# Kernel optimization log

Hardware: AMD Instinct MI355X
Metric: run time of the kernel (lower is better)

Reference implementation:

```python
import jax, jax.numpy as jnp
import numpy as np
import math

C = 384; HQ = 8; HKV = 2; HD = C // HQ; R = 4; L = 4; E = 4; CAPF = 1.25; SCALE = 1.0 / R


def _ln(x, g, b):
    m = jnp.mean(x, -1, keepdims=True)
    v = jnp.mean((x - m) ** 2, -1, keepdims=True)
    return (x - m) * jax.lax.rsqrt(v + 1e-5) * g + b


def _lora(h, W, A, B):
    # base linear (no bias) + low-rank LoRA delta, scale = alpha/r = 0.25
    return h @ W + ((h @ A.T) @ B.T) * SCALE


def _rope(x, cos, sin):
    xe = x[..., 0::2]; xo = x[..., 1::2]
    return jnp.stack((xe * cos - xo * sin, xe * sin + xo * cos), axis=-1).reshape(x.shape)


def _forward(x, adapter_id, ln1_g, ln1_b, ln2_g, ln2_b,
             Wq, Aq, Bq, Wk, Ak, Bk, Wv, Av, Bv, Wo, Ao, Bo,
             Wr, br, W1, A1, B1, W2, A2, B2):
    B, T, _ = x.shape
    aid = adapter_id
    # ---- GQA attention with RoPE ----
    h = _ln(x, ln1_g, ln1_b)
    q = _lora(h, Wq, Aq[aid], Bq[aid]).reshape(B, T, HQ, HD).transpose(0, 2, 1, 3)
    k = _lora(h, Wk, Ak[aid], Bk[aid]).reshape(B, T, HKV, HD).transpose(0, 2, 1, 3)
    v = _lora(h, Wv, Av[aid], Bv[aid]).reshape(B, T, HKV, HD).transpose(0, 2, 1, 3)
    inv = 1.0 / (10000.0 ** (jnp.arange(0, HD, 2, dtype=x.dtype) / HD))
    ang = jnp.arange(T, dtype=x.dtype)[:, None] * inv  # [T, HD/2]
    cos = jnp.cos(ang); sin = jnp.sin(ang)
    q = _rope(q, cos, sin); k = _rope(k, cos, sin)
    rep = HQ // HKV
    k = jnp.repeat(k, rep, axis=1); v = jnp.repeat(v, rep, axis=1)
    s = jnp.einsum('bhqd,bhkd->bhqk', q, k) / math.sqrt(HD)
    causal = jnp.tril(jnp.ones((T, T), dtype=bool))
    s = jnp.where(causal, s, -jnp.inf)
    a = jax.nn.softmax(s, axis=-1)
    o = jnp.einsum('bhqk,bhkd->bhqd', a, v).transpose(0, 2, 1, 3).reshape(B, T, C)
    x = x + _lora(o, Wo, Ao[aid], Bo[aid])
    # ---- capacity-routed top-1 MoE with LoRA FFN experts ----
    flat = _ln(x, ln2_g, ln2_b).reshape(B * T, C)
    probs = jax.nn.softmax(flat @ Wr + br, axis=-1)   # [N, E]
    top1_val = jnp.max(probs, -1)
    top1_idx = jnp.argmax(probs, -1)
    onehot = jax.nn.one_hot(top1_idx, E, dtype=flat.dtype)
    pos = jnp.cumsum(onehot, axis=0) - 1.0            # slot within expert
    cap = int(math.ceil(CAPF * B * T / E))
    dispatch = (pos < cap).astype(flat.dtype) * onehot
    aux = jnp.sum(jnp.mean(probs, 0) * jnp.mean(dispatch, 0)) * E
    posi = pos.astype(jnp.int32)
    # fixed-capacity gather into per-expert buffers (dropped tokens -> slot cap)
    bufs = []
    for e in range(E):
        slot = jnp.where(dispatch[:, e] > 0, posi[:, e], cap)
        bufs.append(jnp.zeros((cap + 1, C), flat.dtype).at[slot].set(flat)[:cap])
    buf = jnp.stack(bufs)                              # [E, cap, C]
    a1 = A1[:, aid]; b1 = B1[:, aid]; a2 = A2[:, aid]; b2 = B2[:, aid]
    h1 = jnp.einsum('enc,eco->eno', buf, W1) \
        + jnp.einsum('enr,eor->eno', jnp.einsum('enc,erc->enr', buf, a1), b1) * SCALE
    h1 = jax.nn.relu(h1)
    o2 = jnp.einsum('enf,efo->eno', h1, W2) \
        + jnp.einsum('enr,eor->eno', jnp.einsum('enf,erf->enr', h1, a2), b2) * SCALE
    out_flat = jnp.zeros_like(flat)
    for e in range(E):
        g = dispatch[:, e] * top1_val                  # gate, zero for undisptched
        out_flat = out_flat + o2[e][jnp.clip(posi[:, e], 0, cap - 1)] * g[:, None]
    return x + out_flat.reshape(B, T, C), aux


def setup_inputs() -> dict:
    key = jax.random.key(0)
    ks = jax.random.split(key, 32)
    B, T = 4, 2048
    n = lambda i, shape, s=0.05: jax.random.normal(ks[i], shape, dtype=jnp.float32) * s
    inp = {
        'x': jax.random.normal(ks[0], (B, T, C), dtype=jnp.float32),
        'adapter_id': 0,
        'ln1_g': jnp.ones((C,), jnp.float32), 'ln1_b': jnp.zeros((C,), jnp.float32),
        'ln2_g': jnp.ones((C,), jnp.float32), 'ln2_b': jnp.zeros((C,), jnp.float32),
        'Wq': n(1, (C, HQ * HD)), 'Aq': n(2, (L, R, C), 0.1), 'Bq': n(3, (L, HQ * HD, R), 0.1),
        'Wk': n(4, (C, HKV * HD)), 'Ak': n(5, (L, R, C), 0.1), 'Bk': n(6, (L, HKV * HD, R), 0.1),
        'Wv': n(7, (C, HKV * HD)), 'Av': n(8, (L, R, C), 0.1), 'Bv': n(9, (L, HKV * HD, R), 0.1),
        'Wo': n(10, (C, C)), 'Ao': n(11, (L, R, C), 0.1), 'Bo': n(12, (L, C, R), 0.1),
        'Wr': n(13, (C, E)), 'br': jnp.zeros((E,), jnp.float32),
        'W1': n(14, (E, C, 4 * C)), 'A1': n(15, (E, L, R, C), 0.1), 'B1': n(16, (E, L, 4 * C, R), 0.1),
        'W2': n(17, (E, 4 * C, C)), 'A2': n(18, (E, L, R, 4 * C), 0.1), 'B2': n(19, (E, L, C, R), 0.1),
    }
    return inp


def reference(x, adapter_id, ln1_g, ln1_b, ln2_g, ln2_b,
              Wq, Aq, Bq, Wk, Ak, Bk, Wv, Av, Bv, Wo, Ao, Bo,
              Wr, br, W1, A1, B1, W2, A2, B2):
    return _forward(x, adapter_id, ln1_g, ln1_b, ln2_g, ln2_b,
                    Wq, Aq, Bq, Wk, Ak, Bk, Wv, Av, Bv, Wo, Ao, Bo,
                    Wr, br, W1, A1, B1, W2, A2, B2)
```

## Files before the change

kernel.cpp:

```cpp
#include <hip/hip_runtime.h>
#include <math.h>

#define NC   384
#define NHQ  8
#define NHKV 2
#define NR   4
#define NEXP 4
#define NB   4
#define NT   2048
#define NTOKENS 8192
#define NCAP 2560
#define NFF  1536
#define NQKV 576
#define LORA_SCALE 0.25f
#define L2E 1.4426950408889634f
#define QSCALE 0.14433756729740643f

#define OB_HSPLIT_HI ((size_t)0)
#define OB_HSPLIT_LO ((size_t)6291456)
#define OB_QHI       ((size_t)12582912)
#define OB_QLO       ((size_t)18874368)
#define OB_KHI       ((size_t)25165824)
#define OB_KLO       ((size_t)26738688)
#define OB_VTHI      ((size_t)28311552)
#define OB_VTLO      ((size_t)29884416)
#define OB_FLAT      ((size_t)31457280)
#define OB_WPKT_HI   ((size_t)44040192)
#define OB_WPKT_LO   ((size_t)44482560)
#define OB_WOET_HI   ((size_t)44924928)
#define OB_WOET_LO   ((size_t)45219840)
#define OB_W1T       ((size_t)45514752)
#define OB_W2T       ((size_t)50233344)
#define OB_PROBS     ((size_t)54951936)
#define OB_T1V       ((size_t)55083008)
#define OB_T1I       ((size_t)55115776)
#define OB_SLOT      ((size_t)55148544)

typedef short bf16x8 __attribute__((ext_vector_type(8)));
typedef float f32x4  __attribute__((ext_vector_type(4)));

__device__ __forceinline__ unsigned short f2bf(float x) {
  union { float f; unsigned u; } a; a.f = x;
  unsigned r = a.u + 0x7FFFu + ((a.u >> 16) & 1u);
  return (unsigned short)(r >> 16);
}
__device__ __forceinline__ float bf2f(unsigned short h) {
  union { unsigned u; float f; } a; a.u = ((unsigned)h) << 16; return a.f;
}

#define MFMA16(a, b, c) __builtin_amdgcn_mfma_f32_16x16x32_bf16((a), (b), (c), 0, 0, 0)

__global__ __launch_bounds__(256) void ln_split_kernel(const float* __restrict__ x,
    const float* __restrict__ g, const float* __restrict__ bb,
    unsigned short* __restrict__ ohi, unsigned short* __restrict__ olo) {
  int row = blockIdx.x * 4 + (threadIdx.x >> 6);
  int lane = threadIdx.x & 63;
  const float* xr = x + (size_t)row * NC;
  float v0[6];
  float s = 0.f;
#pragma unroll
  for (int i = 0; i < 6; i++) { v0[i] = xr[lane + i * 64]; s += v0[i]; }
#pragma unroll
  for (int o = 32; o > 0; o >>= 1) s += __shfl_xor(s, o);
  float mean = s * (1.f / NC);
  float s2 = 0.f;
#pragma unroll
  for (int i = 0; i < 6; i++) { float d = v0[i] - mean; s2 += d * d; }
#pragma unroll
  for (int o = 32; o > 0; o >>= 1) s2 += __shfl_xor(s2, o);
  float rstd = rsqrtf(s2 * (1.f / NC) + 1e-5f);
#pragma unroll
  for (int i = 0; i < 6; i++) {
    int c = lane + i * 64;
    float val = (v0[i] - mean) * rstd * g[c] + bb[c];
    unsigned short h = f2bf(val);
    ohi[(size_t)row * NC + c] = h;
    olo[(size_t)row * NC + c] = f2bf(val - bf2f(h));
  }
}

__global__ __launch_bounds__(256) void ln_kernel(const float* __restrict__ x,
    const float* __restrict__ g, const float* __restrict__ bb,
    float* __restrict__ out) {
  int row = blockIdx.x * 4 + (threadIdx.x >> 6);
  int lane = threadIdx.x & 63;
  const float* xr = x + (size_t)row * NC;
  float v0[6];
  float s = 0.f;
#pragma unroll
  for (int i = 0; i < 6; i++) { v0[i] = xr[lane + i * 64]; s += v0[i]; }
#pragma unroll
  for (int o = 32; o > 0; o >>= 1) s += __shfl_xor(s, o);
  float mean = s * (1.f / NC);
  float s2 = 0.f;
#pragma unroll
  for (int i = 0; i < 6; i++) { float d = v0[i] - mean; s2 += d * d; }
#pragma unroll
  for (int o = 32; o > 0; o >>= 1) s2 += __shfl_xor(s2, o);
  float rstd = rsqrtf(s2 * (1.f / NC) + 1e-5f);
  float* orow = out + (size_t)row * NC;
#pragma unroll
  for (int i = 0; i < 6; i++) {
    int c = lane + i * 64;
    orow[c] = (v0[i] - mean) * rstd * g[c] + bb[c];
  }
}

__global__ __launch_bounds__(256) void pack_attn_kernel(const int* __restrict__ aidp,
    const float* __restrict__ Wq, const float* __restrict__ Aq, const float* __restrict__ Bq,
    const float* __restrict__ Wk, const float* __restrict__ Ak, const float* __restrict__ Bk,
    const float* __restrict__ Wv, const float* __restrict__ Av, const float* __restrict__ Bv,
    const float* __restrict__ Wo, const float* __restrict__ Ao, const float* __restrict__ Bo,
    unsigned short* __restrict__ wpkt_hi, unsigned short* __restrict__ wpkt_lo,
    unsigned short* __restrict__ woet_hi, unsigned short* __restrict__ woet_lo,
    int* __restrict__ slot_token) {
  int aid = aidp[0];
  int idx = blockIdx.x * 256 + threadIdx.x;
  if (idx < NC * NQKV) {
    int c = idx / NQKV, col = idx % NQKV;
    float w; const float* A; const float* B; int loc;
    if (col < 384)      { w = Wq[c * 384 + col];        A = Aq; B = Bq; loc = col; }
    else if (col < 480) { w = Wk[c * 96 + (col - 384)]; A = Ak; B = Bk; loc = col - 384; }
    else                { w = Wv[c * 96 + (col - 480)]; A = Av; B = Bv; loc = col - 480; }
    float s = 0.f;
#pragma unroll
    for (int r = 0; r < 4; r++)
      s += A[((size_t)aid * 4 + r) * NC + c] * B[((size_t)(col < 384 ? aid * 384 : aid * 96) + loc) * 4 + r];
    float val = w + LORA_SCALE * s;
    unsigned short h = f2bf(val);
    size_t tix = (size_t)col * NC + c;
    wpkt_hi[tix] = h; wpkt_lo[tix] = f2bf(val - bf2f(h));
  }
  int j = idx - NC * NQKV;
  if (j >= 0 && j < NC * NC) {
    int c = j / NC, col = j % NC;
    float s = 0.f;
#pragma unroll
    for (int r = 0; r < 4; r++)
      s += Ao[((size_t)aid * 4 + r) * NC + c] * Bo[((size_t)aid * NC + col) * 4 + r];
    float val = Wo[(size_t)c * NC + col] + LORA_SCALE * s;
    unsigned short h = f2bf(val);
    size_t tix = (size_t)col * NC + c;
    woet_hi[tix] = h; woet_lo[tix] = f2bf(val - bf2f(h));
  }
  if (idx < NEXP * NCAP) slot_token[idx] = -1;
}

__global__ __launch_bounds__(256) void pack_w1t_kernel(const int* __restrict__ aidp,
    const float* __restrict__ W1, const float* __restrict__ A1, const float* __restrict__ B1,
    unsigned short* __restrict__ W1T) {
  __shared__ float tile[64][65];
  int aid = aidp[0];
  int e = blockIdx.z, cb = blockIdx.y, fb = blockIdx.x;
  int tid = threadIdx.x;
  int tlo = tid & 63, thi = tid >> 6;
  size_t la = ((size_t)e * 4 + aid);
#pragma unroll
  for (int ii = 0; ii < 16; ii++) {
    int c = cb * 64 + ii * 4 + thi;
    int f = fb * 64 + tlo;
    float val = W1[((size_t)e * NC + c) * NFF + f];
    float s = 0.f;
#pragma unroll
    for (int r = 0; r < 4; r++)
      s += A1[(la * 4 + r) * NC + c] * B1[(la * NFF + f) * 4 + r];
    tile[ii * 4 + thi][tlo] = val + LORA_SCALE * s;
  }
  __syncthreads();
#pragma unroll
  for (int ii = 0; ii < 16; ii++) {
    int floc = ii * 4 + thi;
    W1T[((size_t)e * NFF + fb * 64 + floc) * NC + cb * 64 + tlo] = f2bf(tile[tlo][floc]);
  }
}

__global__ __launch_bounds__(256) void pack_w2t_kernel(const int* __restrict__ aidp,
    const float* __restrict__ W2, const float* __restrict__ A2, const float* __restrict__ B2,
    unsigned short* __restrict__ W2T) {
  __shared__ float tile[64][65];
  int aid = aidp[0];
  int e = blockIdx.z, cb = blockIdx.y, fb = blockIdx.x;
  int tid = threadIdx.x;
  int tlo = tid & 63, thi = tid >> 6;
  size_t la = ((size_t)e * 4 + aid);
#pragma unroll
  for (int ii = 0; ii < 16; ii++) {
    int f = fb * 64 + ii * 4 + thi;
    int c = cb * 64 + tlo;
    float val = W2[((size_t)e * NFF + f) * NC + c];
    float s = 0.f;
#pragma unroll
    for (int r = 0; r < 4; r++)
      s += A2[(la * 4 + r) * NFF + f] * B2[(la * NC + c) * 4 + r];
    tile[ii * 4 + thi][tlo] = val + LORA_SCALE * s;
  }
  __syncthreads();
#pragma unroll
  for (int ii = 0; ii < 16; ii++) {
    int cloc = ii * 4 + thi;
    W2T[((size_t)e * NC + cb * 64 + cloc) * NFF + fb * 64 + tlo] = f2bf(tile[tlo][cloc]);
  }
}

__global__ __launch_bounds__(256) void qkv_mfma_kernel(
    const unsigned short* __restrict__ hhi, const unsigned short* __restrict__ hlo,
    const unsigned short* __restrict__ wthi, const unsigned short* __restrict__ wtlo,
    unsigned short* __restrict__ qhi, unsigned short* __restrict__ qlo,
    unsigned short* __restrict__ khi, unsigned short* __restrict__ klo,
    unsigned short* __restrict__ vthi, unsigned short* __restrict__ vtlo) {
  const int m0 = blockIdx.x * 16;
  const int tid = threadIdx.x;
  const int w = tid >> 6, lane = tid & 63;
  const int lq = lane & 15, g = lane >> 4;
  bf16x8 ah[12], al[12];
  const unsigned short* arow_h = hhi + (size_t)(m0 + lq) * NC;
  const unsigned short* arow_l = hlo + (size_t)(m0 + lq) * NC;
#pragma unroll
  for (int kk = 0; kk < 12; kk++) {
    ah[kk] = *(const bf16x8*)(arow_h + kk * 32 + g * 8);
    al[kk] = *(const bf16x8*)(arow_l + kk * 32 + g * 8);
  }
#pragma unroll
  for (int nt = 0; nt < 9; nt++) {
    const int ncol = w * 144 + nt * 16 + lq;
    const int colbase = w * 144 + nt * 16;
    const unsigned short* bp_h = wthi + (size_t)ncol * NC;
    const unsigned short* bp_l = wtlo + (size_t)ncol * NC;
    f32x4 c = (f32x4){0.f, 0.f, 0.f, 0.f};
#pragma unroll
    for (int kk = 0; kk < 12; kk++) {
      bf16x8 bh = *(const bf16x8*)(bp_h + kk * 32 + g * 8);
      bf16x8 bl = *(const bf16x8*)(bp_l + kk * 32 + g * 8);
      c = MFMA16(ah[kk], bh, c);
      c = MFMA16(al[kk], bh, c);
      c = MFMA16(ah[kk], bl, c);
    }
    if (colbase < 480) {
      const int dloc = ncol % 48;
      const int j = dloc >> 1;
      const int parity = ncol & 1;
      const bool isq = colbase < 384;
      const float scale = isq ? QSCALE : 1.f;
      const float inv = powf(10000.f, -(float)(2 * j) * (1.f / 48.f));
#pragma unroll
      for (int r = 0; r < 4; r++) {
        int row = m0 + g * 4 + r;
        int t = row & (NT - 1);
        int bb = row >> 11;
        float sn, cs; sincosf((float)t * inv, &sn, &cs);
        float pv = __shfl_xor(c[r], 1);
        float roped = (c[r] * cs + (parity ? pv * sn : -pv * sn)) * scale;
        unsigned short h_ = f2bf(roped);
        unsigned short l_ = f2bf(roped - bf2f(h_));
        size_t idx;
        if (isq) {
          idx = ((size_t)(bb * NHQ + ncol / 48) * NT + t) * 48 + dloc;
          qhi[idx] = h_; qlo[idx] = l_;
        } else {
          int ck = ncol - 384;
          idx = ((size_t)(bb * NHKV + ck / 48) * NT + t) * 48 + (ck % 48);
          khi[idx] = h_; klo[idx] = l_;
        }
      }
    } else {
      const int cv = ncol - 480;
      const int hh = cv / 48, dloc = cv % 48;
#pragma unroll
      for (int r = 0; r < 4; r++) {
        int row = m0 + g * 4 + r;
        int t = row & (NT - 1);
        int bb = row >> 11;
        float val = c[r];
        unsigned short h_ = f2bf(val);
        unsigned short l_ = f2bf(val - bf2f(h_));
        size_t idx = ((size_t)(bb * NHKV + hh) * 48 + dloc) * NT + t;
        vthi[idx] = h_; vtlo[idx] = l_;
      }
    }
  }
}

__global__ __launch_bounds__(128) void attn_mfma_kernel(
    const unsigned short* __restrict__ qhi, const unsigned short* __restrict__ qlo,
    const unsigned short* __restrict__ khi, const unsigned short* __restrict__ klo,
    const unsigned short* __restrict__ vthi, const unsigned short* __restrict__ vtlo,
    unsigned short* __restrict__ ohi, unsigned short* __restrict__ olo) {
  __shared__ unsigned short Pt[2][4096];
  const int qb = 31 - (int)blockIdx.x;
  const int bh = blockIdx.y;
  const int b = bh >> 3, hq = bh & 7, hk = hq >> 2;
  const int bhk = b * NHKV + hk;
  const int tid = threadIdx.x;
  const int w = tid >> 6, lane = tid & 63;
  const int lq = lane & 15, g = lane >> 4;
  const int sw = lq & 7;
  unsigned short* PtW = Pt[w];
  const bf16x8 zf = {0, 0, 0, 0, 0, 0, 0, 0};

  bf16x8 qfh[2][2], qfl[2][2];
#pragma unroll
  for (int qs = 0; qs < 2; qs++) {
    size_t qoff = ((size_t)bh * NT + qb * 64 + w * 32 + qs * 16 + lq) * 48;
    qfh[qs][0] = *(const bf16x8*)(qhi + qoff + g * 8);
    qfl[qs][0] = *(const bf16x8*)(qlo + qoff + g * 8);
    qfh[qs][1] = (g < 2) ? *(const bf16x8*)(qhi + qoff + 32 + g * 8) : zf;
    qfl[qs][1] = (g < 2) ? *(const bf16x8*)(qlo + qoff + 32 + g * 8) : zf;
  }
  f32x4 acc[2][3];
#pragma unroll
  for (int qs = 0; qs < 2; qs++)
#pragma unroll
    for (int dt = 0; dt < 3; dt++) acc[qs][dt] = (f32x4){0.f, 0.f, 0.f, 0.f};
  float m[2] = {-1e30f, -1e30f}, l[2] = {0.f, 0.f};

  const unsigned short* kb_h = khi + (size_t)bhk * NT * 48;
  const unsigned short* kb_l = klo + (size_t)bhk * NT * 48;
  const unsigned short* vb_h = vthi + (size_t)bhk * 48 * NT;
  const unsigned short* vb_l = vtlo + (size_t)bhk * 48 * NT;

  for (int kt = 0; kt <= qb; kt++) {
    f32x4 s[2][4];
#pragma unroll
    for (int qs = 0; qs < 2; qs++)
#pragma unroll
      for (int ct = 0; ct < 4; ct++) s[qs][ct] = (f32x4){0.f, 0.f, 0.f, 0.f};
#pragma unroll
    for (int ct = 0; ct < 4; ct++) {
      const size_t ko = (size_t)(kt * 64 + ct * 16 + lq) * 48;
      bf16x8 kh0 = *(const bf16x8*)(kb_h + ko + g * 8);
      bf16x8 kl0 = *(const bf16x8*)(kb_l + ko + g * 8);
      bf16x8 kh1 = (g < 2) ? *(const bf16x8*)(kb_h + ko + 32 + g * 8) : zf;
      bf16x8 kl1 = (g < 2) ? *(const bf16x8*)(kb_l + ko + 32 + g * 8) : zf;
#pragma unroll
      for (int qs = 0; qs < 2; qs++) {
        s[qs][ct] = MFMA16(kh0, qfh[qs][0], s[qs][ct]);
        s[qs][ct] = MFMA16(kl0, qfh[qs][0], s[qs][ct]);
        s[qs][ct] = MFMA16(kh0, qfl[qs][0], s[qs][ct]);
        s[qs][ct] = MFMA16(kh1, qfh[qs][1], s[qs][ct]);
        s[qs][ct] = MFMA16(kl1, qfh[qs][1], s[qs][ct]);
        s[qs][ct] = MFMA16(kh1, qfl[qs][1], s[qs][ct]);
      }
    }
    if (kt == qb) {
#pragma unroll
      for (int qs = 0; qs < 2; qs++) {
        const int qg = qb * 64 + w * 32 + qs * 16 + lq;
#pragma unroll
        for (int ct = 0; ct < 4; ct++) {
          const int k0 = kt * 64 + ct * 16 + g * 4;
#pragma unroll
          for (int r = 0; r < 4; r++)
            if (k0 + r > qg) s[qs][ct][r] = -1e30f;
        }
      }
    }
#pragma unroll
    for (int qs = 0; qs < 2; qs++) {
      float mx = s[qs][0][0];
#pragma unroll
      for (int ct = 0; ct < 4; ct++)
#pragma unroll
        for (int r = 0; r < 4; r++) mx = fmaxf(mx, s[qs][ct][r]);
      mx = fmaxf(mx, __shfl_xor(mx, 16));
      mx = fmaxf(mx, __shfl_xor(mx, 32));
      const float mnew = fmaxf(m[qs], mx);
      const float corr = exp2f((m[qs] - mnew) * L2E);
      m[qs] = mnew;
      float ps = 0.f;
      unsigned short* prow = PtW + (qs * 16 + lq) * 128;
#pragma unroll
      for (int ct = 0; ct < 4; ct++) {
        float p0 = exp2f((s[qs][ct][0] - mnew) * L2E);
        float p1 = exp2f((s[qs][ct][1] - mnew) * L2E);
        float p2 = exp2f((s[qs][ct][2] - mnew) * L2E);
        float p3 = exp2f((s[qs][ct][3] - mnew) * L2E);
        ps += (p0 + p1) + (p2 + p3);
        unsigned short h0 = f2bf(p0), h1 = f2bf(p1), h2 = f2bf(p2), h3 = f2bf(p3);
        unsigned short l0 = f2bf(p0 - bf2f(h0)), l1 = f2bf(p1 - bf2f(h1));
        unsigned short l2 = f2bf(p2 - bf2f(h2)), l3 = f2bf(p3 - bf2f(h3));
        uint2 wh, wl;
        wh.x = (unsigned)h0 | ((unsigned)h1 << 16); wh.y = (unsigned)h2 | ((unsigned)h3 << 16);
        wl.x = (unsigned)l0 | ((unsigned)l1 << 16); wl.y = (unsigned)l2 | ((unsigned)l3 << 16);
        const int u = ct * 2 + (g >> 1), sub = (g & 1) * 4;
        *(uint2*)&prow[((u ^ sw) << 3) + sub] = wh;
        *(uint2*)&prow[(((8 + u) ^ sw) << 3) + sub] = wl;
      }
      ps += __shfl_xor(ps, 16);
      ps += __shfl_xor(ps, 32);
      l[qs] = l[qs] * corr + ps;
#pragma unroll
      for (int dt = 0; dt < 3; dt++) acc[qs][dt] *= corr;
    }
    bf16x8 pfh[2][2], pfl[2][2];
#pragma unroll
    for (int qs = 0; qs < 2; qs++) {
      const unsigned short* prow = PtW + (qs * 16 + lq) * 128;
#pragma unroll
      for (int c = 0; c < 2; c++) {
        pfh[qs][c] = *(const bf16x8*)&prow[((c * 4 + g) ^ sw) << 3];
        pfl[qs][c] = *(const bf16x8*)&prow[((8 + c * 4 + g) ^ sw) << 3];
      }
    }
#pragma unroll
    for (int dt = 0; dt < 3; dt++) {
      const size_t vo = (size_t)(dt * 16 + lq) * NT + kt * 64;
      bf16x8 vh0 = *(const bf16x8*)(vb_h + vo + g * 8);
      bf16x8 vl0 = *(const bf16x8*)(vb_l + vo + g * 8);
      bf16x8 vh1 = *(const bf16x8*)(vb_h + vo + 32 + g * 8);
      bf16x8 vl1 = *(const bf16x8*)(vb_l + vo + 32 + g * 8);
#pragma unroll
      for (int qs = 0; qs < 2; qs++) {
        acc[qs][dt] = MFMA16(vh0, pfh[qs][0], acc[qs][dt]);
        acc[qs][dt] = MFMA16(vl0, pfh[qs][0], acc[qs][dt]);
        acc[qs][dt] = MFMA16(vh0, pfl[qs][0], acc[qs][dt]);
        acc[qs][dt] = MFMA16(vh1, pfh[qs][1], acc[qs][dt]);
        acc[qs][dt] = MFMA16(vl1, pfh[qs][1], acc[qs][dt]);
        acc[qs][dt] = MFMA16(vh1, pfl[qs][1], acc[qs][dt]);
      }
    }
  }
#pragma unroll
  for (int qs = 0; qs < 2; qs++) {
    const float invl = 1.f / l[qs];
    const int qg = qb * 64 + w * 32 + qs * 16 + lq;
    const size_t base = ((size_t)b * NT + qg) * NC + hq * 48 + g * 4;
#pragma unroll
    for (int dt = 0; dt < 3; dt++) {
      unsigned short h4[4], l4[4];
#pragma unroll
      for (int r = 0; r < 4; r++) {
        float v = acc[qs][dt][r] * invl;
        h4[r] = f2bf(v);
        l4[r] = f2bf(v - bf2f(h4[r]));
      }
      uint2 wh, wl;
      wh.x = (unsigned)h4[0] | ((unsigned)h4[1] << 16); wh.y = (unsigned)h4[2] | ((unsigned)h4[3] << 16);
      wl.x = (unsigned)l4[0] | ((unsigned)l4[1] << 16); wl.y = (unsigned)l4[2] | ((unsigned)l4[3] << 16);
      *(uint2*)(ohi + base + dt * 16) = wh;
      *(uint2*)(olo + base + dt * 16) = wl;
    }
  }
}

__global__ __launch_bounds__(256) void proj_mfma_kernel(
    const unsigned short* __restrict__ ohi, const unsigned short* __restrict__ olo,
    const unsigned short* __restrict__ wthi, const unsigned short* __restrict__ wtlo,
    const float* __restrict__ x, float* __restrict__ out) {
  const int m0 = blockIdx.x * 16;
  const int tid = threadIdx.x;
  const int w = tid >> 6, lane = tid & 63;
  const int lq = lane & 15, g = lane >> 4;
  bf16x8 ah[12], al[12];
  const unsigned short* arow_h = ohi + (size_t)(m0 + lq) * NC;
  const unsigned short* arow_l = olo + (size_t)(m0 + lq) * NC;
#pragma unroll
  for (int kk = 0; kk < 12; kk++) {
    ah[kk] = *(const bf16x8*)(arow_h + kk * 32 + g * 8);
    al[kk] = *(const bf16x8*)(arow_l + kk * 32 + g * 8);
  }
#pragma unroll
  for (int nt = 0; nt < 6; nt++) {
    const int ncol = w * 96 + nt * 16 + lq;
    const unsigned short* bp_h = wthi + (size_t)ncol * NC;
    const unsigned short* bp_l = wtlo + (size_t)ncol * NC;
    f32x4 c = (f32x4){0.f, 0.f, 0.f, 0.f};
#pragma unroll
    for (int kk = 0; kk < 12; kk++) {
      bf16x8 bh = *(const bf16x8*)(bp_h + kk * 32 + g * 8);
      bf16x8 bl = *(const bf16x8*)(bp_l + kk * 32 + g * 8);
      c = MFMA16(ah[kk], bh, c);
      c = MFMA16(al[kk], bh, c);
      c = MFMA16(ah[kk], bl, c);
    }
#pragma unroll
    for (int r = 0; r < 4; r++) {
      size_t row = m0 + g * 4 + r;
      out[row * NC + ncol] = x[row * NC + ncol] + c[r];
    }
  }
}

__global__ __launch_bounds__(256) void router_kernel(const float* __restrict__ flat,
    const float* __restrict__ Wr, const float* __restrict__ br,
    float* __restrict__ probs, float* __restrict__ top1_val, int* __restrict__ top1_idx) {
  int tid = threadIdx.x;
  int lane = tid & 63, w = tid >> 6;
  int token = blockIdx.x * 4 + w;
  const float* fr = flat + (size_t)token * NC;
  float p0 = 0.f, p1 = 0.f, p2 = 0.f, p3 = 0.f;
  for (int c = lane; c < NC; c += 64) {
    float f = fr[c];
    const float4 wr = *(const float4*)(Wr + c * 4);
    p0 += f * wr.x; p1 += f * wr.y; p2 += f * wr.z; p3 += f * wr.w;
  }
#pragma unroll
  for (int off = 32; off > 0; off >>= 1) {
    p0 += __shfl_xor(p0, off); p1 += __shfl_xor(p1, off);
    p2 += __shfl_xor(p2, off); p3 += __shfl_xor(p3, off);
  }
  if (lane == 0) {
    float l0 = p0 + br[0], l1 = p1 + br[1], l2 = p2 + br[2], l3 = p3 + br[3];
    float mx = fmaxf(fmaxf(l0, l1), fmaxf(l2, l3));
    float e0 = expf(l0 - mx), e1 = expf(l1 - mx), e2 = expf(l2 - mx), e3 = expf(l3 - mx);
    float inv = 1.f / (e0 + e1 + e2 + e3);
    float q0 = e0 * inv, q1 = e1 * inv, q2 = e2 * inv, q3 = e3 * inv;
    probs[token * 4 + 0] = q0; probs[token * 4 + 1] = q1;
    probs[token * 4 + 2] = q2; probs[token * 4 + 3] = q3;
    int best = 0; float bv = q0;
    if (q1 > bv) { bv = q1; best = 1; }
    if (q2 > bv) { bv = q2; best = 2; }
    if (q3 > bv) { bv = q3; best = 3; }
    top1_idx[token] = best;
    top1_val[token] = bv;
  }
}

__global__ __launch_bounds__(256) void scan_kernel(const int* __restrict__ top1_idx,
    const float* __restrict__ probs, int* __restrict__ slot_token,
    float* __restrict__ aux_out) {
  __shared__ float psums[4];
  __shared__ int cnts[4][256];
  __shared__ int tot[4];
  int tid = threadIdx.x;
  int base = tid * 32;
  float s0 = 0.f, s1 = 0.f, s2 = 0.f, s3 = 0.f;
  int c0 = 0, c1 = 0, c2 = 0, c3 = 0;
  for (int i = 0; i < 32; i++) {
    int tk = base + i;
    s0 += probs[tk * 4 + 0]; s1 += probs[tk * 4 + 1];
    s2 += probs[tk * 4 + 2]; s3 += probs[tk * 4 + 3];
    int e = top1_idx[tk];
    if (e == 0) c0++; else if (e == 1) c1++; else if (e == 2) c2++; else c3++;
  }
  if (tid < 4) psums[tid] = 0.f;
  cnts[0][tid] = c0; cnts[1][tid] = c1; cnts[2][tid] = c2; cnts[3][tid] = c3;
  __syncthreads();
#pragma unroll
  for (int off = 32; off > 0; off >>= 1) {
    s0 += __shfl_xor(s0, off); s1 += __shfl_xor(s1, off);
    s2 += __shfl_xor(s2, off); s3 += __shfl_xor(s3, off);
  }
  if ((tid & 63) == 0) {
    atomicAdd(&psums[0], s0); atomicAdd(&psums[1], s1);
    atomicAdd(&psums[2], s2); atomicAdd(&psums[3], s3);
  }
  int w = tid >> 6, lane = tid & 63;
  int v0 = cnts[w][lane * 4 + 0], v1 = cnts[w][lane * 4 + 1];
  int v2 = cnts[w][lane * 4 + 2], v3 = cnts[w][lane * 4 + 3];
  int t4 = v0 + v1 + v2 + v3;
  int incl = t4;
#pragma unroll
  for (int off = 1; off < 64; off <<= 1) {
    int n = __shfl_up(incl, off);
    if (lane >= off) incl += n;
  }
  int excl = incl - t4;
  __syncthreads();
  cnts[w][lane * 4 + 0] = excl;
  cnts[w][lane * 4 + 1] = excl + v0;
  cnts[w][lane * 4 + 2] = excl + v0 + v1;
  cnts[w][lane * 4 + 3] = excl + v0 + v1 + v2;
  if (lane == 63) tot[w] = incl;
  __syncthreads();
  int pe0 = cnts[0][tid], pe1 = cnts[1][tid], pe2 = cnts[2][tid], pe3 = cnts[3][tid];
  for (int i = 0; i < 32; i++) {
    int tk = base + i;
    int e = top1_idx[tk];
    int r;
    if (e == 0) r = pe0++;
    else if (e == 1) r = pe1++;
    else if (e == 2) r = pe2++;
    else r = pe3++;
    if (r < NCAP) slot_token[e * NCAP + r] = tk;
  }
  __syncthreads();
  if (tid == 0) {
    float aux = 0.f;
#pragma unroll
    for (int e = 0; e < 4; e++) {
      int d = tot[e] < NCAP ? tot[e] : NCAP;
      aux += (psums[e] * (1.f / NTOKENS)) * ((float)d * (1.f / NTOKENS));
    }
    aux_out[0] = aux * (float)NEXP;
  }
}

__global__ __launch_bounds__(256) void ffn_mfma_kernel(const float* __restrict__ flat,
    const int* __restrict__ slot_token, const float* __restrict__ top1_val,
    const unsigned short* __restrict__ W1T, const unsigned short* __restrict__ W2T,
    float* __restrict__ out) {
  __shared__ unsigned short ft[32][392];
  __shared__ unsigned short hc[32][520];
  __shared__ int toks[32];
  __shared__ float gates[32];
  int e = blockIdx.y;
  int s0 = blockIdx.x * 32;
  int tid = threadIdx.x;
  int w = tid >> 6, lane = tid & 63;
  int row_a = lane & 15;
  int kgrp = lane >> 4;
  if (tid < 32) {
    int tk = slot_token[e * NCAP + s0 + tid];
    toks[tid] = tk;
    gates[tid] = (tk >= 0) ? top1_val[tk] : 0.f;
  }
  __syncthreads();
  if (toks[0] < 0) return;
  for (int i = tid; i < 32 * 384; i += 256) {
    int r = i / 384, c = i - r * 384;
    int tk = toks[r];
    float xv = (tk >= 0) ? flat[(size_t)tk * NC + c] : 0.f;
    ft[r][c] = f2bf(xv);
  }
  __syncthreads();
  f32x4 acc2[2][6];
#pragma unroll
  for (int mt = 0; mt < 2; mt++)
#pragma unroll
    for (int nt = 0; nt < 6; nt++) acc2[mt][nt] = (f32x4){0.f, 0.f, 0.f, 0.f};

  for (int ch = 0; ch < 3; ch++) {
#pragma unroll
    for (int mt = 0; mt < 2; mt++) {
      bf16x8 a[12];
#pragma unroll
      for (int kk = 0; kk < 12; kk++)
        a[kk] = *(const bf16x8*)&ft[mt * 16 + row_a][kk * 32 + kgrp * 8];
#pragma unroll
      for (int nt = 0; nt < 8; nt++) {
        int ncol = ch * 512 + w * 128 + nt * 16 + row_a;
        const unsigned short* bp = W1T + ((size_t)e * NFF + ncol) * NC;
        f32x4 c = (f32x4){0.f, 0.f, 0.f, 0.f};
#pragma unroll
        for (int kk = 0; kk < 12; kk++) {
          bf16x8 bf = *(const bf16x8*)(bp + kk * 32 + kgrp * 8);
          c = MFMA16(a[kk], bf, c);
        }
        int hcol = w * 128 + nt * 16 + row_a;
#pragma unroll
        for (int r = 0; r < 4; r++) {
          hc[mt * 16 + kgrp * 4 + r][hcol] = f2bf(fmaxf(c[r], 0.f));
        }
      }
    }
    __syncthreads();
#pragma unroll
    for (int mt = 0; mt < 2; mt++) {
      bf16x8 a2[16];
#pragma unroll
      for (int kk = 0; kk < 16; kk++)
        a2[kk] = *(const bf16x8*)&hc[mt * 16 + row_a][kk * 32 + kgrp * 8];
#pragma unroll
      for (int nt = 0; nt < 6; nt++) {
        int ncol = w * 96 + nt * 16 + row_a;
        const unsigned short* bp = W2T + ((size_t)e * NC + ncol) * NFF + ch * 512;
        f32x4 c = acc2[mt][nt];
#pragma unroll
        for (int kk = 0; kk < 16; kk++) {
          bf16x8 bf = *(const bf16x8*)(bp + kk * 32 + kgrp * 8);
          c = MFMA16(a2[kk], bf, c);
        }
        acc2[mt][nt] = c;
      }
    }
    __syncthreads();
  }
#pragma unroll
  for (int mt = 0; mt < 2; mt++) {
#pragma unroll
    for (int r = 0; r < 4; r++) {
      int srow = mt * 16 + kgrp * 4 + r;
      int tk = toks[srow];
      if (tk < 0) continue;
      float g = gates[srow];
#pragma unroll
      for (int nt = 0; nt < 6; nt++) {
        int col = w * 96 + nt * 16 + row_a;
        out[(size_t)tk * NC + col] += acc2[mt][nt][r] * g;
      }
    }
  }
}

extern "C" void kernel_launch(void* const* d_in, const int* in_sizes, int n_in,
                              void* d_out, int out_size, void* d_ws, size_t ws_size,
                              hipStream_t stream) {
  const float* x   = (const float*)d_in[0];
  const int*   aid = (const int*)d_in[1];
  const float* ln1g = (const float*)d_in[2];
  const float* ln1b = (const float*)d_in[3];
  const float* ln2g = (const float*)d_in[4];
  const float* ln2b = (const float*)d_in[5];
  const float* Wq = (const float*)d_in[6];
  const float* Aq = (const float*)d_in[7];
  const float* Bq = (const float*)d_in[8];
  const float* Wk = (const float*)d_in[9];
  const float* Ak = (const float*)d_in[10];
  const float* Bk = (const float*)d_in[11];
  const float* Wv = (const float*)d_in[12];
  const float* Av = (const float*)d_in[13];
  const float* Bv = (const float*)d_in[14];
  const float* Wo = (const float*)d_in[15];
  const float* Ao = (const float*)d_in[16];
  const float* Bo = (const float*)d_in[17];
  const float* Wr = (const float*)d_in[18];
  const float* br = (const float*)d_in[19];
  const float* W1 = (const float*)d_in[20];
  const float* A1 = (const float*)d_in[21];
  const float* B1 = (const float*)d_in[22];
  const float* W2 = (const float*)d_in[23];
  const float* A2 = (const float*)d_in[24];
  const float* B2 = (const float*)d_in[25];
  float* out = (float*)d_out;
  char* wsb = (char*)d_ws;

  unsigned short* hhi  = (unsigned short*)(wsb + OB_HSPLIT_HI);
  unsigned short* hlo  = (unsigned short*)(wsb + OB_HSPLIT_LO);
  unsigned short* ohi  = (unsigned short*)(wsb + OB_HSPLIT_HI);
  unsigned short* olo  = (unsigned short*)(wsb + OB_HSPLIT_LO);
  unsigned short* qhi  = (unsigned short*)(wsb + OB_QHI);
  unsigned short* qlo  = (unsigned short*)(wsb + OB_QLO);
  unsigned short* khi  = (unsigned short*)(wsb + OB_KHI);
  unsigned short* klo  = (unsigned short*)(wsb + OB_KLO);
  unsigned short* vthi = (unsigned short*)(wsb + OB_VTHI);
  unsigned short* vtlo = (unsigned short*)(wsb + OB_VTLO);
  float* flat          = (float*)(wsb + OB_FLAT);
  unsigned short* wpkt_hi = (unsigned short*)(wsb + OB_WPKT_HI);
  unsigned short* wpkt_lo = (unsigned short*)(wsb + OB_WPKT_LO);
  unsigned short* woet_hi = (unsigned short*)(wsb + OB_WOET_HI);
  unsigned short* woet_lo = (unsigned short*)(wsb + OB_WOET_LO);
  unsigned short* W1T  = (unsigned short*)(wsb + OB_W1T);
  unsigned short* W2T  = (unsigned short*)(wsb + OB_W2T);
  float* probs         = (float*)(wsb + OB_PROBS);
  float* t1v           = (float*)(wsb + OB_T1V);
  int*   t1i           = (int*)(wsb + OB_T1I);
  int*   slot          = (int*)(wsb + OB_SLOT);

  pack_attn_kernel<<<1440, 256, 0, stream>>>(aid, Wq, Aq, Bq, Wk, Ak, Bk, Wv, Av, Bv,
                                             Wo, Ao, Bo, wpkt_hi, wpkt_lo, woet_hi, woet_lo, slot);
  pack_w1t_kernel<<<dim3(24, 6, 4), 256, 0, stream>>>(aid, W1, A1, B1, W1T);
  pack_w2t_kernel<<<dim3(24, 6, 4), 256, 0, stream>>>(aid, W2, A2, B2, W2T);
  ln_split_kernel<<<NTOKENS / 4, 256, 0, stream>>>(x, ln1g, ln1b, hhi, hlo);
  qkv_mfma_kernel<<<NTOKENS / 16, 256, 0, stream>>>(hhi, hlo, wpkt_hi, wpkt_lo,
                                                    qhi, qlo, khi, klo, vthi, vtlo);
  attn_mfma_kernel<<<dim3(32, 32), 128, 0, stream>>>(qhi, qlo, khi, klo, vthi, vtlo, ohi, olo);
  proj_mfma_kernel<<<NTOKENS / 16, 256, 0, stream>>>(ohi, olo, woet_hi, woet_lo, x, out);
  ln_kernel<<<NTOKENS / 4, 256, 0, stream>>>(out, ln2g, ln2b, flat);
  router_kernel<<<NTOKENS / 4, 256, 0, stream>>>(flat, Wr, br, probs, t1v, t1i);
  scan_kernel<<<1, 256, 0, stream>>>(t1i, probs, slot, out + (size_t)NTOKENS * NC);
  ffn_mfma_kernel<<<dim3(NCAP / 32, NEXP), 256, 0, stream>>>(flat, slot, t1v, W1T, W2T, out);
}
```

Before: 694.0 us.

## Split fused MoE FFN into two kernels with a bf16 hidden buffer

Replaces the single fused FFN kernel, which kept the 1536-wide hidden chunk in shared memory and ran 320 blocks, with two kernels. The first computes the ReLU hidden activations into a global bf16 buffer and is spread over six column tiles per slot block. The second reads that buffer and does the down projection over two output halves. This exposes far more blocks to fill the GPU, at the cost of a global round-trip for the hidden activations (about 31MB written and read). The second kernel also reads its A operand straight from global memory without going through LDS.

```diff
diff --git a/kernel.cpp b/kernel.cpp
--- a/kernel.cpp
+++ b/kernel.cpp
@@ -24,6 +24,7 @@
 #define OB_KLO       ((size_t)26738688)
 #define OB_VTHI      ((size_t)28311552)
 #define OB_VTLO      ((size_t)29884416)
+#define OB_H1        ((size_t)0)
 #define OB_FLAT      ((size_t)31457280)
 #define OB_WPKT_HI   ((size_t)44040192)
 #define OB_WPKT_LO   ((size_t)44482560)
@@ -585,25 +586,19 @@
   }
 }
 
-__global__ __launch_bounds__(256) void ffn_mfma_kernel(const float* __restrict__ flat,
-    const int* __restrict__ slot_token, const float* __restrict__ top1_val,
-    const unsigned short* __restrict__ W1T, const unsigned short* __restrict__ W2T,
-    float* __restrict__ out) {
+__global__ __launch_bounds__(256) void ffn1_kernel(const float* __restrict__ flat,
+    const int* __restrict__ slot_token,
+    const unsigned short* __restrict__ W1T,
+    unsigned short* __restrict__ h1) {
   __shared__ unsigned short ft[32][392];
-  __shared__ unsigned short hc[32][520];
   __shared__ int toks[32];
-  __shared__ float gates[32];
-  int e = blockIdx.y;
-  int s0 = blockIdx.x * 32;
-  int tid = threadIdx.x;
-  int w = tid >> 6, lane = tid & 63;
-  int row_a = lane & 15;
-  int kgrp = lane >> 4;
-  if (tid < 32) {
-    int tk = slot_token[e * NCAP + s0 + tid];
-    toks[tid] = tk;
-    gates[tid] = (tk >= 0) ? top1_val[tk] : 0.f;
-  }
+  const int e = blockIdx.z;
+  const int n0 = blockIdx.y * 256;
+  const int s0 = blockIdx.x * 32;
+  const int tid = threadIdx.x;
+  const int w = tid >> 6, lane = tid & 63;
+  const int lq = lane & 15, kgrp = lane >> 4;
+  if (tid < 32) toks[tid] = slot_token[e * NCAP + s0 + tid];
   __syncthreads();
   if (toks[0] < 0) return;
   for (int i = tid; i < 32 * 384; i += 256) {
@@ -613,70 +608,90 @@
     ft[r][c] = f2bf(xv);
   }
   __syncthreads();
-  f32x4 acc2[2][6];
+  bf16x8 a[2][12];
 #pragma unroll
   for (int mt = 0; mt < 2; mt++)
 #pragma unroll
-    for (int nt = 0; nt < 6; nt++) acc2[mt][nt] = (f32x4){0.f, 0.f, 0.f, 0.f};
-
-  for (int ch = 0; ch < 3; ch++) {
-#pragma unroll
-    for (int mt = 0; mt < 2; mt++) {
-      bf16x8 a[12];
-#pragma unroll
-      for (int kk = 0; kk < 12; kk++)
-        a[kk] = *(const bf16x8*)&ft[mt * 16 + row_a][kk * 32 + kgrp * 8];
-#pragma unroll
-      for (int nt = 0; nt < 8; nt++) {
-        int ncol = ch * 512 + w * 128 + nt * 16 + row_a;
-        const unsigned short* bp = W1T + ((size_t)e * NFF + ncol) * NC;
-        f32x4 c = (f32x4){0.f, 0.f, 0.f, 0.f};
-#pragma unroll
-        for (int kk = 0; kk < 12; kk++) {
-          bf16x8 bf = *(const bf16x8*)(bp + kk * 32 + kgrp * 8);
-          c = MFMA16(a[kk], bf, c);
-        }
-        int hcol = w * 128 + nt * 16 + row_a;
-#pragma unroll
-        for (int r = 0; r < 4; r++) {
-          hc[mt * 16 + kgrp * 4 + r][hcol] = f2bf(fmaxf(c[r], 0.f));
-        }
-      }
-    }
-    __syncthreads();
-#pragma unroll
-    for (int mt = 0; mt < 2; mt++) {
-      bf16x8 a2[16];
-#pragma unroll
-      for (int kk = 0; kk < 16; kk++)
-        a2[kk] = *(const bf16x8*)&hc[mt * 16 + row_a][kk * 32 + kgrp * 8];
-#pragma unroll
-      for (int nt = 0; nt < 6; nt++) {
-        int ncol = w * 96 + nt * 16 + row_a;
-        const unsigned short* bp = W2T + ((size_t)e * NC + ncol) * NFF + ch * 512;
-        f32x4 c = acc2[mt][nt];
-#pragma unroll
-        for (int kk = 0; kk < 16; kk++) {
-          bf16x8 bf = *(const bf16x8*)(bp + kk * 32 + kgrp * 8);
-          c = MFMA16(a2[kk], bf, c);
-        }
-        acc2[mt][nt] = c;
-      }
-    }
-    __syncthreads();
+    for (int kk = 0; kk < 12; kk++)
+      a[mt][kk] = *(const bf16x8*)&ft[mt * 16 + lq][kk * 32 + kgrp * 8];
+#pragma unroll
+  for (int nt = 0; nt < 4; nt++) {
+    const int ncol = n0 + w * 64 + nt * 16 + lq;
+    const unsigned short* bp = W1T + ((size_t)e * NFF + ncol) * NC;
+    f32x4 c0 = (f32x4){0.f, 0.f, 0.f, 0.f};
+    f32x4 c1 = (f32x4){0.f, 0.f, 0.f, 0.f};
+#pragma unroll
+    for (int kk = 0; kk < 12; kk++) {
+      bf16x8 bf = *(const bf16x8*)(bp + kk * 32 + kgrp * 8);
+      c0 = MFMA16(a[0][kk], bf, c0);
+      c1 = MFMA16(a[1][kk], bf, c1);
+    }
+    unsigned short* hp0 = h1 + ((size_t)(e * NCAP + s0 + kgrp * 4)) * NFF + ncol;
+    unsigned short* hp1 = hp0 + (size_t)16 * NFF;
+#pragma unroll
+    for (int r = 0; r < 4; r++) {
+      hp0[(size_t)r * NFF] = f2bf(fmaxf(c0[r], 0.f));
+      hp1[(size_t)r * NFF] = f2bf(fmaxf(c1[r], 0.f));
+    }
+  }
+}
+
+__global__ __launch_bounds__(256) void ffn2_kernel(
+    const int* __restrict__ slot_token, const float* __restrict__ top1_val,
+    const unsigned short* __restrict__ h1, const unsigned short* __restrict__ W2T,
+    float* __restrict__ out) {
+  __shared__ int toks[32];
+  __shared__ float gates[32];
+  const int e = blockIdx.z;
+  const int nh = blockIdx.y;
+  const int s0 = blockIdx.x * 32;
+  const int tid = threadIdx.x;
+  const int w = tid >> 6, lane = tid & 63;
+  const int lq = lane & 15, kgrp = lane >> 4;
+  if (tid < 32) {
+    int tk = slot_token[e * NCAP + s0 + tid];
+    toks[tid] = tk;
+    gates[tid] = (tk >= 0) ? top1_val[tk] : 0.f;
+  }
+  __syncthreads();
+  if (toks[0] < 0) return;
+  const unsigned short* a0p = h1 + ((size_t)(e * NCAP + s0 + lq)) * NFF + kgrp * 8;
+  const unsigned short* a1p = a0p + (size_t)16 * NFF;
+  const int ncb = nh * 192 + w * 48;
+  const unsigned short* bp0 = W2T + ((size_t)e * NC + ncb + lq) * NFF + kgrp * 8;
+  const unsigned short* bp1 = bp0 + (size_t)16 * NFF;
+  const unsigned short* bp2 = bp0 + (size_t)32 * NFF;
+  f32x4 acc[2][3];
+#pragma unroll
+  for (int mt = 0; mt < 2; mt++)
+#pragma unroll
+    for (int nt = 0; nt < 3; nt++) acc[mt][nt] = (f32x4){0.f, 0.f, 0.f, 0.f};
+#pragma unroll 8
+  for (int kk = 0; kk < 48; kk++) {
+    bf16x8 af0 = *(const bf16x8*)(a0p + kk * 32);
+    bf16x8 af1 = *(const bf16x8*)(a1p + kk * 32);
+    bf16x8 b0 = *(const bf16x8*)(bp0 + kk * 32);
+    bf16x8 b1 = *(const bf16x8*)(bp1 + kk * 32);
+    bf16x8 b2 = *(const bf16x8*)(bp2 + kk * 32);
+    acc[0][0] = MFMA16(af0, b0, acc[0][0]);
+    acc[1][0] = MFMA16(af1, b0, acc[1][0]);
+    acc[0][1] = MFMA16(af0, b1, acc[0][1]);
+    acc[1][1] = MFMA16(af1, b1, acc[1][1]);
+    acc[0][2] = MFMA16(af0, b2, acc[0][2]);
+    acc[1][2] = MFMA16(af1, b2, acc[1][2]);
   }
 #pragma unroll
   for (int mt = 0; mt < 2; mt++) {
 #pragma unroll
     for (int r = 0; r < 4; r++) {
-      int srow = mt * 16 + kgrp * 4 + r;
-      int tk = toks[srow];
+      const int srow = mt * 16 + kgrp * 4 + r;
+      const int tk = toks[srow];
       if (tk < 0) continue;
-      float g = gates[srow];
-#pragma unroll
-      for (int nt = 0; nt < 6; nt++) {
-        int col = w * 96 + nt * 16 + row_a;
-        out[(size_t)tk * NC + col] += acc2[mt][nt][r] * g;
+      const float g = gates[srow];
+#pragma unroll
+      for (int nt = 0; nt < 3; nt++) {
+        const int col = ncb + nt * 16 + lq;
+        out[(size_t)tk * NC + col] += acc[mt][nt][r] * g;
       }
     }
   }
@@ -724,6 +739,7 @@
   unsigned short* klo  = (unsigned short*)(wsb + OB_KLO);
   unsigned short* vthi = (unsigned short*)(wsb + OB_VTHI);
   unsigned short* vtlo = (unsigned short*)(wsb + OB_VTLO);
+  unsigned short* h1   = (unsigned short*)(wsb + OB_H1);
   float* flat          = (float*)(wsb + OB_FLAT);
   unsigned short* wpkt_hi = (unsigned short*)(wsb + OB_WPKT_HI);
   unsigned short* wpkt_lo = (unsigned short*)(wsb + OB_WPKT_LO);
@@ -748,5 +764,6 @@
   ln_kernel<<<NTOKENS / 4, 256, 0, stream>>>(out, ln2g, ln2b, flat);
   router_kernel<<<NTOKENS / 4, 256, 0, stream>>>(flat, Wr, br, probs, t1v, t1i);
   scan_kernel<<<1, 256, 0, stream>>>(t1i, probs, slot, out + (size_t)NTOKENS * NC);
-  ffn_mfma_kernel<<<dim3(NCAP / 32, NEXP), 256, 0, stream>>>(flat, slot, t1v, W1T, W2T, out);
-}
+  ffn1_kernel<<<dim3(NCAP / 32, NFF / 256, NEXP), 256, 0, stream>>>(flat, slot, W1T, h1);
+  ffn2_kernel<<<dim3(NCAP / 32, 2, NEXP), 256, 0, stream>>>(slot, t1v, h1, W2T, out);
+}
```

After: 627.8 us. 9.5% less time.
